# Optimization experiments

Hardware: AMD Instinct MI355X
Metric: run time of the kernel (lower is better)

Reference implementation:

```python
import jax, jax.numpy as jnp
import numpy as np

B, H, M, HS = 256, 1024, 256, 128  # batch, hidden=entry_size, mem_cap, head_size
TAU = 1.0
sg = jax.lax.stop_gradient


def _gumbel(u):
    # torch: -log(1e-20 - log(1e-20 + rand))
    return -jnp.log(1e-20 - jnp.log(1e-20 + u))


def _hard_gumbel_softmax(scores, u, tau):
    # straight-through hard gumbel softmax over the memcap axis (axis=1)
    y = jax.nn.softmax((scores + sg(_gumbel(u))) * tau, axis=1)
    ymax = jnp.max(y, axis=1, keepdims=True)
    hard = (y == ymax).astype(y.dtype)
    return sg(hard - y) + y


def setup_inputs() -> dict:
    key = jax.random.key(0)
    ks = jax.random.split(key, 20)
    stdv = 1.0 / np.sqrt(H)
    U = lambda k, shp: jax.random.uniform(k, shp, jnp.float32, -stdv, stdv)
    inp = {
        'input_': jax.random.normal(ks[0], (B, H), jnp.float32),
        'h_0': jax.random.normal(ks[1], (B, H), jnp.float32),
        'mem': jnp.zeros((B, M, H), jnp.float32),
        'last_usage': jnp.full((B, M), -99999.0, jnp.float32),
        'u1': jax.random.uniform(ks[2], (B, M), jnp.float32),
        'u2': jax.random.uniform(ks[3], (B, M), jnp.float32),
        'W_ih': U(ks[4], (H, 3 * H)),
        'W_hh': U(ks[5], (H, 3 * H)),
        'W_rh': U(ks[6], (H, 3 * H)),
        'W_s1': U(ks[7], (H, H)),
        'W_s2': U(ks[8], (H, H)),
        'W_s3': U(ks[9], (H, H)),
        'bias': jnp.zeros((1, 3 * H), jnp.float32),
        'W_im': U(ks[10], (H, HS + 1)),
        'W_hm': U(ks[11], (H, HS + 1)),
        'fc1_w': U(ks[12], (HS, H)),
        'fc1_b': jnp.zeros((HS,), jnp.float32),
        'W_im1': U(ks[13], (H, HS + 1)),
        'W_hm1': U(ks[14], (H, HS + 1)),
        'W_mm1': U(ks[15], (H, HS + 1)),
        'bias_m1': jnp.zeros((1, HS + 1), jnp.float32),
        'bias_1': jnp.zeros((1, H), jnp.float32),
        'bias_2': jnp.zeros((1, H), jnp.float32),
        'bias_3': jnp.zeros((1, H), jnp.float32),
    }
    return inp


def reference(input_, h_0, mem, last_usage, u1, u2,
              W_ih, W_hh, W_rh, W_s1, W_s2, W_s3, bias,
              W_im, W_hm, fc1_w, fc1_b,
              W_im1, W_hm1, W_mm1, bias_m1, bias_1, bias_2, bias_3):
    memcap = mem.shape[1]
    hidden = h_0.shape[1]
    # write: memcnt == 0 -> one-hot write index at slot 0, broadcast over batch
    widx = jnp.zeros((1, memcap), mem.dtype).at[0, 0].set(1.0)
    ones = widx[:, :, None]                       # (1, M, 1)
    mem = h_0[:, None, :] * ones + mem * (1.0 - ones)  # (B, M, E)
    last_use = jax.nn.sigmoid(sg(last_usage))     # (B, M), detached
    # addressing head (computed on detached input/h_0/mem, as in torch)
    read_head = jnp.tanh(sg(input_) @ W_im + sg(h_0) @ W_hm)          # (B, HS+1)
    head_vecs = jnp.concatenate(
        [sg(mem) @ fc1_w.T + fc1_b, last_use[:, :, None]], axis=2)    # (B, M, HS+1)
    scores = jnp.einsum('bh,bmh->bm', read_head, head_vecs)
    y1 = _hard_gumbel_softmax(scores, u1, TAU)
    entry = jnp.einsum('bm,bme->be', y1, mem)     # (B, E)
    # GRU-like gating
    w_b = jax.nn.sigmoid(entry @ W_rh + h_0 @ W_hh + input_ @ W_ih + bias)
    r, z, n = jnp.split(w_b, 3, axis=1)
    h_new = jnp.tanh(input_ @ W_s1 + bias_1 + r * (h_0 @ W_s2 + bias_2)
                     + z * (bias_3 + entry @ W_s3))
    # second read head (not detached)
    head1 = jnp.tanh(input_ @ W_im1 + h_0 @ W_hm1 + entry @ W_mm1 + bias_m1)
    scores1 = jnp.einsum('bh,bmh->bm', head1, head_vecs)
    y2 = _hard_gumbel_softmax(scores1, u2, TAU)
    entry_o = jnp.einsum('bm,bme->be', y2, mem)
    h_1 = n * h_new + (1.0 - n) * h_0
    o = jnp.concatenate([h_1, entry_o], axis=1)
    return (h_1, o)
```

## Files before the change

### kernel.cpp

```cpp
#include <hip/hip_runtime.h>

#define BB 256
#define HH 1024
#define MM 256
#define HS 128
#define NH 129

typedef __attribute__((ext_vector_type(8))) short short8;
typedef __attribute__((ext_vector_type(4))) float float4v;

__device__ __forceinline__ float sigmoidf_(float x) { return 1.0f / (1.0f + expf(-x)); }
__device__ __forceinline__ float gumbelf_(float u) { return -logf(1e-20f - logf(1e-20f + u)); }

__device__ __forceinline__ unsigned short f2bf(float x) {
    union { float f; unsigned u; } c; c.f = x;
    unsigned u = c.u;
    return (unsigned short)((u + 0x7FFFu + ((u >> 16) & 1u)) >> 16);
}

__global__ __launch_bounds__(256) void k_cvt_w(const float* __restrict__ W_ih,
                                               const float* __restrict__ W_hh,
                                               const float* __restrict__ W_rh,
                                               const float* __restrict__ W_s1,
                                               const float* __restrict__ W_s2,
                                               const float* __restrict__ W_s3,
                                               unsigned short* __restrict__ WtG,
                                               unsigned short* __restrict__ WtS) {
    __shared__ unsigned short T[64][66];
    int bx = blockIdx.x;
    const float* src;
    unsigned short* dst;
    int k0, n0, sstr, dstr, krel;
    if (bx < 2304) {
        int kt = bx / 48, nt = bx % 48;
        k0 = kt * 64; n0 = nt * 64;
        src = (k0 < 1024) ? W_ih : (k0 < 2048) ? W_hh : W_rh;
        krel = k0 & 1023;
        dst = WtG; sstr = 3072; dstr = 3072;
    } else {
        int r = bx - 2304;
        int seg = r >> 8;
        int rem = r & 255;
        int kt = rem >> 4, nt = rem & 15;
        k0 = kt * 64; n0 = nt * 64;
        src = (seg == 0) ? W_s1 : (seg == 1) ? W_s2 : W_s3;
        krel = k0;
        dst = WtS + (size_t)seg * 1048576; sstr = 1024; dstr = 1024;
    }
    int t = threadIdx.x;
    for (int i = 0; i < 4; ++i) {
        int e = i * 256 + t;
        int kk = e >> 4, nn0 = (e & 15) * 4;
        float4 v = *(const float4*)(src + (size_t)(krel + kk) * sstr + n0 + nn0);
        T[nn0 + 0][kk] = f2bf(v.x);
        T[nn0 + 1][kk] = f2bf(v.y);
        T[nn0 + 2][kk] = f2bf(v.z);
        T[nn0 + 3][kk] = f2bf(v.w);
    }
    __syncthreads();
    for (int i = 0; i < 8; ++i) {
        int e = i * 256 + t;
        int nn = e >> 5, kk2 = (e & 31) * 2;
        unsigned val = (unsigned)T[nn][kk2] | ((unsigned)T[nn][kk2 + 1] << 16);
        *(unsigned*)(dst + (size_t)(n0 + nn) * dstr + k0 + kk2) = val;
    }
}

__global__ __launch_bounds__(1024) void k_score1(const float* __restrict__ input_,
                                                 const float* __restrict__ h0,
                                                 const float* __restrict__ W_im,
                                                 const float* __restrict__ W_hm,
                                                 const float* __restrict__ fc1_w,
                                                 const float* __restrict__ fc1_b,
                                                 const float* __restrict__ mem,
                                                 const float* __restrict__ last_usage,
                                                 const float* __restrict__ u1,
                                                 unsigned short* __restrict__ Abf,
                                                 float* __restrict__ sg_out) {
    __shared__ float sx[HH], sh[HH], sv[HH];
    __shared__ float red[8][128];
    __shared__ float red2[8];
    __shared__ float sj[NH];
    __shared__ float scb;
    int b = blockIdx.x, t = threadIdx.x;
    if (t < 256) {
        float4 v = *(const float4*)(input_ + (size_t)b * HH + t * 4);
        *(float4*)(sx + t * 4) = v;
        ushort4 o; o.x = f2bf(v.x); o.y = f2bf(v.y); o.z = f2bf(v.z); o.w = f2bf(v.w);
        *(ushort4*)(Abf + (size_t)b * 3072 + t * 4) = o;
    } else if (t < 512) {
        int tt = t - 256;
        float4 v = *(const float4*)(h0 + (size_t)b * HH + tt * 4);
        *(float4*)(sh + tt * 4) = v;
        ushort4 o; o.x = f2bf(v.x); o.y = f2bf(v.y); o.z = f2bf(v.z); o.w = f2bf(v.w);
        *(ushort4*)(Abf + (size_t)b * 3072 + 1024 + tt * 4) = o;
    }
    __syncthreads();
    {
        int j = t & 127, ks = t >> 7;
        int hb = ks * 128;
        float p = 0.f;
#pragma unroll 8
        for (int h = hb; h < hb + 128; ++h)
            p += sx[h] * W_im[h * NH + j] + sh[h] * W_hm[h * NH + j];
        red[ks][j] = p;
        if (t >= 1016) {
            int k2 = t - 1016;
            int hb2 = k2 * 128;
            float q = 0.f;
#pragma unroll 8
            for (int h = hb2; h < hb2 + 128; ++h)
                q += sx[h] * W_im[h * NH + 128] + sh[h] * W_hm[h * NH + 128];
            red2[k2] = q;
        }
    }
    __syncthreads();
    if (t < 128) {
        float s = 0.f;
        for (int k = 0; k < 8; ++k) s += red[k][t];
        sj[t] = tanhf(s);
    } else if (t == 128) {
        float s = 0.f;
        for (int k = 0; k < 8; ++k) s += red2[k];
        sj[128] = tanhf(s);
    }
    __syncthreads();
    {
        float acc = 0.f;
#pragma unroll 4
        for (int j = 0; j < HS; ++j) acc += sj[j] * fc1_w[(size_t)j * HH + t];
        sv[t] = acc;
    }
    if (t < 64) {
        float p = sj[t] * fc1_b[t] + sj[t + 64] * fc1_b[t + 64];
        for (int off = 32; off > 0; off >>= 1) p += __shfl_down(p, off, 64);
        if (t == 0) scb = p;
    }
    __syncthreads();
    float cb = scb, hf = sj[128];
    int wave = t >> 6, lane = t & 63;
    float4 rv[4];
#pragma unroll
    for (int it = 0; it < 4; ++it) rv[it] = *(const float4*)(sv + it * 256 + lane * 4);
    for (int i = 0; i < 16; ++i) {
        int m = wave * 16 + i;
        const float* row = (m == 0) ? (h0 + (size_t)b * HH) : (mem + ((size_t)(b * MM + m)) * HH);
        float p = 0.f;
#pragma unroll
        for (int it = 0; it < 4; ++it) {
            float4 mv = *(const float4*)(row + it * 256 + lane * 4);
            p += mv.x * rv[it].x + mv.y * rv[it].y + mv.z * rv[it].z + mv.w * rv[it].w;
        }
        for (int off = 32; off > 0; off >>= 1) p += __shfl_down(p, off, 64);
        if (lane == 0) {
            float lu = sigmoidf_(last_usage[b * MM + m]);
            sg_out[b * MM + m] = p + cb + hf * lu + gumbelf_(u1[b * MM + m]);
        }
    }
}

__global__ __launch_bounds__(1024) void k_sel_score2(const float* __restrict__ sg1,
                                                     const float* __restrict__ mem,
                                                     const float* __restrict__ h0,
                                                     const float* __restrict__ input_,
                                                     const float* __restrict__ W_im1,
                                                     const float* __restrict__ W_hm1,
                                                     const float* __restrict__ W_mm1,
                                                     const float* __restrict__ bias_m1,
                                                     const float* __restrict__ fc1_w,
                                                     const float* __restrict__ fc1_b,
                                                     const float* __restrict__ last_usage,
                                                     const float* __restrict__ u2,
                                                     unsigned short* __restrict__ Abf,
                                                     float* __restrict__ sg_out) {
    __shared__ float svals[256];
    __shared__ int sidx[256];
    __shared__ float sx[HH], sh[HH], se[HH], sv[HH];
    __shared__ float red[8][128];
    __shared__ float red2[8];
    __shared__ float sj[NH];
    __shared__ float scb;
    int b = blockIdx.x, t = threadIdx.x;
    if (t < 256) {
        svals[t] = sg1[b * MM + t];
        sidx[t] = t;
    }
    __syncthreads();
    for (int s = 128; s > 0; s >>= 1) {
        if (t < s) {
            if (svals[t + s] > svals[t]) { svals[t] = svals[t + s]; sidx[t] = sidx[t + s]; }
        }
        __syncthreads();
    }
    int mstar = sidx[0];
    const float* erow = (mstar == 0) ? (h0 + (size_t)b * HH) : (mem + ((size_t)(b * MM + mstar)) * HH);
    if (t < 256) {
        float4 v = *(const float4*)(erow + t * 4);
        *(float4*)(se + t * 4) = v;
        ushort4 o; o.x = f2bf(v.x); o.y = f2bf(v.y); o.z = f2bf(v.z); o.w = f2bf(v.w);
        *(ushort4*)(Abf + (size_t)b * 3072 + 2048 + t * 4) = o;
    } else if (t < 512) {
        int tt = t - 256;
        *(float4*)(sx + tt * 4) = *(const float4*)(input_ + (size_t)b * HH + tt * 4);
    } else if (t < 768) {
        int tt = t - 512;
        *(float4*)(sh + tt * 4) = *(const float4*)(h0 + (size_t)b * HH + tt * 4);
    }
    __syncthreads();
    {
        int j = t & 127, ks = t >> 7;
        int hb = ks * 128;
        float p = 0.f;
#pragma unroll 4
        for (int h = hb; h < hb + 128; ++h)
            p += sx[h] * W_im1[h * NH + j] + sh[h] * W_hm1[h * NH + j] + se[h] * W_mm1[h * NH + j];
        red[ks][j] = p;
        if (t >= 1016) {
            int k2 = t - 1016;
            int hb2 = k2 * 128;
            float q = 0.f;
#pragma unroll 4
            for (int h = hb2; h < hb2 + 128; ++h)
                q += sx[h] * W_im1[h * NH + 128] + sh[h] * W_hm1[h * NH + 128] + se[h] * W_mm1[h * NH + 128];
            red2[k2] = q;
        }
    }
    __syncthreads();
    if (t < 128) {
        float s = bias_m1[t];
        for (int k = 0; k < 8; ++k) s += red[k][t];
        sj[t] = tanhf(s);
    } else if (t == 128) {
        float s = bias_m1[128];
        for (int k = 0; k < 8; ++k) s += red2[k];
        sj[128] = tanhf(s);
    }
    __syncthreads();
    {
        float acc = 0.f;
#pragma unroll 4
        for (int j = 0; j < HS; ++j) acc += sj[j] * fc1_w[(size_t)j * HH + t];
        sv[t] = acc;
    }
    if (t < 64) {
        float p = sj[t] * fc1_b[t] + sj[t + 64] * fc1_b[t + 64];
        for (int off = 32; off > 0; off >>= 1) p += __shfl_down(p, off, 64);
        if (t == 0) scb = p;
    }
    __syncthreads();
    float cb = scb, hf = sj[128];
    int wave = t >> 6, lane = t & 63;
    float4 rv[4];
#pragma unroll
    for (int it = 0; it < 4; ++it) rv[it] = *(const float4*)(sv + it * 256 + lane * 4);
    for (int i = 0; i < 16; ++i) {
        int m = wave * 16 + i;
        const float* row = (m == 0) ? (h0 + (size_t)b * HH) : (mem + ((size_t)(b * MM + m)) * HH);
        float p = 0.f;
#pragma unroll
        for (int it = 0; it < 4; ++it) {
            float4 mv = *(const float4*)(row + it * 256 + lane * 4);
            p += mv.x * rv[it].x + mv.y * rv[it].y + mv.z * rv[it].z + mv.w * rv[it].w;
        }
        for (int off = 32; off > 0; off >>= 1) p += __shfl_down(p, off, 64);
        if (lane == 0) {
            float lu = sigmoidf_(last_usage[b * MM + m]);
            sg_out[b * MM + m] = p + cb + hf * lu + gumbelf_(u2[b * MM + m]);
        }
    }
}

__global__ __launch_bounds__(256) void k_gemm(const unsigned short* __restrict__ Abf,
                                              const unsigned short* __restrict__ WtG,
                                              const unsigned short* __restrict__ WtS,
                                              float* __restrict__ wbp,
                                              float* __restrict__ Sp) {
    __shared__ unsigned short As[128 * 72];
    __shared__ unsigned short Bs[128 * 72];
    int bx = blockIdx.x;
    int mtile = bx & 1, unit = bx >> 1;
    int m0 = mtile * 128;
    const unsigned short* Bp;
    const unsigned short* Ap;
    float* pout;
    int bstr, ncol0;
    if (unit < 144) {
        int nt = unit % 24;
        int kidx = unit / 24;
        int ksel = kidx >> 1, khalf = kidx & 1;
        ncol0 = nt * 128;
        Bp = WtG + (size_t)ncol0 * 3072 + ksel * 1024 + khalf * 512;
        bstr = 3072;
        Ap = Abf + ksel * 1024 + khalf * 512;
        pout = wbp + (size_t)kidx * 786432;
    } else {
        int su = unit - 144;
        int seg = su / 16;
        int rem = su % 16;
        int khalf = rem >> 3, nts = rem & 7;
        ncol0 = seg * 1024 + nts * 128;
        Bp = WtS + (size_t)seg * 1048576 + (size_t)(nts * 128) * 1024 + khalf * 512;
        bstr = 1024;
        Ap = Abf + seg * 1024 + khalf * 512;
        pout = Sp + (size_t)khalf * 786432;
    }

    int tid = threadIdx.x;
    int wave = tid >> 6, lane = tid & 63;
    int wm = wave >> 1, wn = wave & 1;
    int q = lane >> 4, lm = lane & 15;

    float4v acc[4][4];
    for (int i = 0; i < 4; ++i)
        for (int j = 0; j < 4; ++j)
            acc[i][j] = (float4v){0.f, 0.f, 0.f, 0.f};

    for (int kt = 0; kt < 512; kt += 64) {
        for (int rr = 0; rr < 4; ++rr) {
            int e = rr * 256 + tid;
            int row = e >> 3, cg = e & 7;
            *(uint4*)&As[row * 72 + cg * 8] =
                *(const uint4*)(Ap + (size_t)(m0 + row) * 3072 + kt + cg * 8);
            *(uint4*)&Bs[row * 72 + cg * 8] =
                *(const uint4*)(Bp + (size_t)row * bstr + kt + cg * 8);
        }
        __syncthreads();
        for (int ks = 0; ks < 64; ks += 32) {
            short8 av[4], bv[4];
            for (int i = 0; i < 4; ++i)
                av[i] = *(const short8*)&As[(wm * 64 + i * 16 + lm) * 72 + ks + q * 8];
            for (int j = 0; j < 4; ++j)
                bv[j] = *(const short8*)&Bs[(wn * 64 + j * 16 + lm) * 72 + ks + q * 8];
            for (int i = 0; i < 4; ++i)
                for (int j = 0; j < 4; ++j)
                    acc[i][j] = __builtin_amdgcn_mfma_f32_16x16x32_bf16(av[i], bv[j], acc[i][j], 0, 0, 0);
        }
        __syncthreads();
    }

    for (int i = 0; i < 4; ++i)
        for (int j = 0; j < 4; ++j) {
            int n = ncol0 + wn * 64 + j * 16 + lm;
            for (int reg = 0; reg < 4; ++reg) {
                int m = m0 + wm * 64 + i * 16 + q * 4 + reg;
                pout[(size_t)m * 3072 + n] = acc[i][j][reg];
            }
        }
}

__global__ __launch_bounds__(256) void k_final(const float* __restrict__ sg2,
                                               const float* __restrict__ mem,
                                               const float* __restrict__ wbp,
                                               const float* __restrict__ Sp,
                                               const float* __restrict__ h0,
                                               const float* __restrict__ bias,
                                               const float* __restrict__ b1,
                                               const float* __restrict__ b2,
                                               const float* __restrict__ b3,
                                               float* __restrict__ out) {
    __shared__ float svals[256];
    __shared__ int sidx[256];
    int b = blockIdx.x, t = threadIdx.x;
    svals[t] = sg2[b * MM + t];
    sidx[t] = t;
    __syncthreads();
    for (int s = 128; s > 0; s >>= 1) {
        if (t < s) {
            if (svals[t + s] > svals[t]) { svals[t] = svals[t + s]; sidx[t] = sidx[t + s]; }
        }
        __syncthreads();
    }
    int mstar = sidx[0];
    const float* erow = (mstar == 0) ? (h0 + (size_t)b * HH) : (mem + ((size_t)(b * MM + mstar)) * HH);
    float* o_row = out + (size_t)BB * HH + (size_t)b * 2 * HH;
    {
        int hb = t * 4;
        *(float4*)(o_row + HH + hb) = *(const float4*)(erow + hb);
    }
    int h = t * 4;
    size_t base = (size_t)b * 3072;
// ... 53 lines not shown
    const float* h0 = (const float*)d_in[1];
    const float* mem = (const float*)d_in[2];
    const float* last_usage = (const float*)d_in[3];
    const float* u1 = (const float*)d_in[4];
    const float* u2 = (const float*)d_in[5];
    const float* W_ih = (const float*)d_in[6];
    const float* W_hh = (const float*)d_in[7];
    const float* W_rh = (const float*)d_in[8];
    const float* W_s1 = (const float*)d_in[9];
    const float* W_s2 = (const float*)d_in[10];
    const float* W_s3 = (const float*)d_in[11];
    const float* bias = (const float*)d_in[12];
    const float* W_im = (const float*)d_in[13];
    const float* W_hm = (const float*)d_in[14];
    const float* fc1_w = (const float*)d_in[15];
    const float* fc1_b = (const float*)d_in[16];
    const float* W_im1 = (const float*)d_in[17];
    const float* W_hm1 = (const float*)d_in[18];
    const float* W_mm1 = (const float*)d_in[19];
    const float* bias_m1 = (const float*)d_in[20];
    const float* bias_1 = (const float*)d_in[21];
    const float* bias_2 = (const float*)d_in[22];
    const float* bias_3 = (const float*)d_in[23];
    float* out = (float*)d_out;

    float* ws = (float*)d_ws;
    float* sg1 = ws;
    float* sg2 = sg1 + 65536;
    float* wbp = sg2 + 65536;
    float* Sp = wbp + 6 * 786432;
    unsigned short* Abf = (unsigned short*)(Sp + 2 * 786432);
    unsigned short* WtG = Abf + 786432;
    unsigned short* WtS = WtG + 9437184;

    k_cvt_w<<<3072, 256, 0, stream>>>(W_ih, W_hh, W_rh, W_s1, W_s2, W_s3, WtG, WtS);
    k_score1<<<BB, 1024, 0, stream>>>(input_, h0, W_im, W_hm, fc1_w, fc1_b,
                                      mem, last_usage, u1, Abf, sg1);
    k_sel_score2<<<BB, 1024, 0, stream>>>(sg1, mem, h0, input_, W_im1, W_hm1, W_mm1, bias_m1,
                                          fc1_w, fc1_b, last_usage, u2, Abf, sg2);
    k_gemm<<<384, 256, 0, stream>>>(Abf, WtG, WtS, wbp, Sp);
    k_final<<<BB, 256, 0, stream>>>(sg2, mem, wbp, Sp, h0, bias, bias_1, bias_2, bias_3, out);
}
```

Before: 595.9 us.

## Fuse weight conversion with score1 and overlap input/h0 GEMMs with score2

Merges the bf16 weight transpose-conversion into the first scoring kernel as extra blocks, so both run in one launch. The second-scoring kernel also carries the GEMM tiles for the input and h0 K-slices, which do not depend on the selected entry, so they run alongside the selection work. Only the entry-dependent K-slices stay in a smaller follow-up GEMM launch. Scoring blocks shrink from 1024 to 256 threads with more work per thread, which cuts per-block parallelism in exchange for co-scheduling. There is a risk that the phase-2 GEMM blocks read WtG/WtS right after phase 1 writes them, but they are in separate launches on the same stream, so ordering holds.

```diff
diff --git a/kernel.cpp b/kernel.cpp
--- a/kernel.cpp
+++ b/kernel.cpp
@@ -18,293 +18,11 @@
     return (unsigned short)((u + 0x7FFFu + ((u >> 16) & 1u)) >> 16);
 }
 
-__global__ __launch_bounds__(256) void k_cvt_w(const float* __restrict__ W_ih,
-                                               const float* __restrict__ W_hh,
-                                               const float* __restrict__ W_rh,
-                                               const float* __restrict__ W_s1,
-                                               const float* __restrict__ W_s2,
-                                               const float* __restrict__ W_s3,
-                                               unsigned short* __restrict__ WtG,
-                                               unsigned short* __restrict__ WtS) {
-    __shared__ unsigned short T[64][66];
-    int bx = blockIdx.x;
-    const float* src;
-    unsigned short* dst;
-    int k0, n0, sstr, dstr, krel;
-    if (bx < 2304) {
-        int kt = bx / 48, nt = bx % 48;
-        k0 = kt * 64; n0 = nt * 64;
-        src = (k0 < 1024) ? W_ih : (k0 < 2048) ? W_hh : W_rh;
-        krel = k0 & 1023;
-        dst = WtG; sstr = 3072; dstr = 3072;
-    } else {
-        int r = bx - 2304;
-        int seg = r >> 8;
-        int rem = r & 255;
-        int kt = rem >> 4, nt = rem & 15;
-        k0 = kt * 64; n0 = nt * 64;
-        src = (seg == 0) ? W_s1 : (seg == 1) ? W_s2 : W_s3;
-        krel = k0;
-        dst = WtS + (size_t)seg * 1048576; sstr = 1024; dstr = 1024;
-    }
-    int t = threadIdx.x;
-    for (int i = 0; i < 4; ++i) {
-        int e = i * 256 + t;
-        int kk = e >> 4, nn0 = (e & 15) * 4;
-        float4 v = *(const float4*)(src + (size_t)(krel + kk) * sstr + n0 + nn0);
-        T[nn0 + 0][kk] = f2bf(v.x);
-        T[nn0 + 1][kk] = f2bf(v.y);
-        T[nn0 + 2][kk] = f2bf(v.z);
-        T[nn0 + 3][kk] = f2bf(v.w);
-    }
-    __syncthreads();
-    for (int i = 0; i < 8; ++i) {
-        int e = i * 256 + t;
-        int nn = e >> 5, kk2 = (e & 31) * 2;
-        unsigned val = (unsigned)T[nn][kk2] | ((unsigned)T[nn][kk2 + 1] << 16);
-        *(unsigned*)(dst + (size_t)(n0 + nn) * dstr + k0 + kk2) = val;
-    }
-}
-
-__global__ __launch_bounds__(1024) void k_score1(const float* __restrict__ input_,
-                                                 const float* __restrict__ h0,
-                                                 const float* __restrict__ W_im,
-                                                 const float* __restrict__ W_hm,
-                                                 const float* __restrict__ fc1_w,
-                                                 const float* __restrict__ fc1_b,
-                                                 const float* __restrict__ mem,
-                                                 const float* __restrict__ last_usage,
-                                                 const float* __restrict__ u1,
-                                                 unsigned short* __restrict__ Abf,
-                                                 float* __restrict__ sg_out) {
-    __shared__ float sx[HH], sh[HH], sv[HH];
-    __shared__ float red[8][128];
-    __shared__ float red2[8];
-    __shared__ float sj[NH];
-    __shared__ float scb;
-    int b = blockIdx.x, t = threadIdx.x;
-    if (t < 256) {
-        float4 v = *(const float4*)(input_ + (size_t)b * HH + t * 4);
-        *(float4*)(sx + t * 4) = v;
-        ushort4 o; o.x = f2bf(v.x); o.y = f2bf(v.y); o.z = f2bf(v.z); o.w = f2bf(v.w);
-        *(ushort4*)(Abf + (size_t)b * 3072 + t * 4) = o;
-    } else if (t < 512) {
-        int tt = t - 256;
-        float4 v = *(const float4*)(h0 + (size_t)b * HH + tt * 4);
-        *(float4*)(sh + tt * 4) = v;
-        ushort4 o; o.x = f2bf(v.x); o.y = f2bf(v.y); o.z = f2bf(v.z); o.w = f2bf(v.w);
-        *(ushort4*)(Abf + (size_t)b * 3072 + 1024 + tt * 4) = o;
-    }
-    __syncthreads();
-    {
-        int j = t & 127, ks = t >> 7;
-        int hb = ks * 128;
-        float p = 0.f;
-#pragma unroll 8
-        for (int h = hb; h < hb + 128; ++h)
-            p += sx[h] * W_im[h * NH + j] + sh[h] * W_hm[h * NH + j];
-        red[ks][j] = p;
-        if (t >= 1016) {
-            int k2 = t - 1016;
-            int hb2 = k2 * 128;
-            float q = 0.f;
-#pragma unroll 8
-            for (int h = hb2; h < hb2 + 128; ++h)
-                q += sx[h] * W_im[h * NH + 128] + sh[h] * W_hm[h * NH + 128];
-            red2[k2] = q;
-        }
-    }
-    __syncthreads();
-    if (t < 128) {
-        float s = 0.f;
-        for (int k = 0; k < 8; ++k) s += red[k][t];
-        sj[t] = tanhf(s);
-    } else if (t == 128) {
-        float s = 0.f;
-        for (int k = 0; k < 8; ++k) s += red2[k];
-        sj[128] = tanhf(s);
-    }
-    __syncthreads();
-    {
-        float acc = 0.f;
-#pragma unroll 4
-        for (int j = 0; j < HS; ++j) acc += sj[j] * fc1_w[(size_t)j * HH + t];
-        sv[t] = acc;
-    }
-    if (t < 64) {
-        float p = sj[t] * fc1_b[t] + sj[t + 64] * fc1_b[t + 64];
-        for (int off = 32; off > 0; off >>= 1) p += __shfl_down(p, off, 64);
-        if (t == 0) scb = p;
-    }
-    __syncthreads();
-    float cb = scb, hf = sj[128];
-    int wave = t >> 6, lane = t & 63;
-    float4 rv[4];
-#pragma unroll
-    for (int it = 0; it < 4; ++it) rv[it] = *(const float4*)(sv + it * 256 + lane * 4);
-    for (int i = 0; i < 16; ++i) {
-        int m = wave * 16 + i;
-        const float* row = (m == 0) ? (h0 + (size_t)b * HH) : (mem + ((size_t)(b * MM + m)) * HH);
-        float p = 0.f;
-#pragma unroll
-        for (int it = 0; it < 4; ++it) {
-            float4 mv = *(const float4*)(row + it * 256 + lane * 4);
-            p += mv.x * rv[it].x + mv.y * rv[it].y + mv.z * rv[it].z + mv.w * rv[it].w;
-        }
-        for (int off = 32; off > 0; off >>= 1) p += __shfl_down(p, off, 64);
-        if (lane == 0) {
-            float lu = sigmoidf_(last_usage[b * MM + m]);
-            sg_out[b * MM + m] = p + cb + hf * lu + gumbelf_(u1[b * MM + m]);
-        }
-    }
-}
-
-__global__ __launch_bounds__(1024) void k_sel_score2(const float* __restrict__ sg1,
-                                                     const float* __restrict__ mem,
-                                                     const float* __restrict__ h0,
-                                                     const float* __restrict__ input_,
-                                                     const float* __restrict__ W_im1,
-                                                     const float* __restrict__ W_hm1,
-                                                     const float* __restrict__ W_mm1,
-                                                     const float* __restrict__ bias_m1,
-                                                     const float* __restrict__ fc1_w,
-                                                     const float* __restrict__ fc1_b,
-                                                     const float* __restrict__ last_usage,
-                                                     const float* __restrict__ u2,
-                                                     unsigned short* __restrict__ Abf,
-                                                     float* __restrict__ sg_out) {
-    __shared__ float svals[256];
-    __shared__ int sidx[256];
-    __shared__ float sx[HH], sh[HH], se[HH], sv[HH];
-    __shared__ float red[8][128];
-    __shared__ float red2[8];
-    __shared__ float sj[NH];
-    __shared__ float scb;
-    int b = blockIdx.x, t = threadIdx.x;
-    if (t < 256) {
-        svals[t] = sg1[b * MM + t];
-        sidx[t] = t;
-    }
-    __syncthreads();
-    for (int s = 128; s > 0; s >>= 1) {
-        if (t < s) {
-            if (svals[t + s] > svals[t]) { svals[t] = svals[t + s]; sidx[t] = sidx[t + s]; }
-        }
-        __syncthreads();
-    }
-    int mstar = sidx[0];
-    const float* erow = (mstar == 0) ? (h0 + (size_t)b * HH) : (mem + ((size_t)(b * MM + mstar)) * HH);
-    if (t < 256) {
-        float4 v = *(const float4*)(erow + t * 4);
-        *(float4*)(se + t * 4) = v;
-        ushort4 o; o.x = f2bf(v.x); o.y = f2bf(v.y); o.z = f2bf(v.z); o.w = f2bf(v.w);
-        *(ushort4*)(Abf + (size_t)b * 3072 + 2048 + t * 4) = o;
-    } else if (t < 512) {
-        int tt = t - 256;
-        *(float4*)(sx + tt * 4) = *(const float4*)(input_ + (size_t)b * HH + tt * 4);
-    } else if (t < 768) {
-        int tt = t - 512;
-        *(float4*)(sh + tt * 4) = *(const float4*)(h0 + (size_t)b * HH + tt * 4);
-    }
-    __syncthreads();
-    {
-        int j = t & 127, ks = t >> 7;
-        int hb = ks * 128;
-        float p = 0.f;
-#pragma unroll 4
-        for (int h = hb; h < hb + 128; ++h)
-            p += sx[h] * W_im1[h * NH + j] + sh[h] * W_hm1[h * NH + j] + se[h] * W_mm1[h * NH + j];
-        red[ks][j] = p;
-        if (t >= 1016) {
-            int k2 = t - 1016;
-            int hb2 = k2 * 128;
-            float q = 0.f;
-#pragma unroll 4
-            for (int h = hb2; h < hb2 + 128; ++h)
-                q += sx[h] * W_im1[h * NH + 128] + sh[h] * W_hm1[h * NH + 128] + se[h] * W_mm1[h * NH + 128];
-            red2[k2] = q;
-        }
-    }
-    __syncthreads();
-    if (t < 128) {
-        float s = bias_m1[t];
-        for (int k = 0; k < 8; ++k) s += red[k][t];
-        sj[t] = tanhf(s);
-    } else if (t == 128) {
-        float s = bias_m1[128];
-        for (int k = 0; k < 8; ++k) s += red2[k];
-        sj[128] = tanhf(s);
-    }
-    __syncthreads();
-    {
-        float acc = 0.f;
-#pragma unroll 4
-        for (int j = 0; j < HS; ++j) acc += sj[j] * fc1_w[(size_t)j * HH + t];
-        sv[t] = acc;
-    }
-    if (t < 64) {
-        float p = sj[t] * fc1_b[t] + sj[t + 64] * fc1_b[t + 64];
-        for (int off = 32; off > 0; off >>= 1) p += __shfl_down(p, off, 64);
-        if (t == 0) scb = p;
-    }
-    __syncthreads();
-    float cb = scb, hf = sj[128];
-    int wave = t >> 6, lane = t & 63;
-    float4 rv[4];
-#pragma unroll
-    for (int it = 0; it < 4; ++it) rv[it] = *(const float4*)(sv + it * 256 + lane * 4);
-    for (int i = 0; i < 16; ++i) {
-        int m = wave * 16 + i;
-        const float* row = (m == 0) ? (h0 + (size_t)b * HH) : (mem + ((size_t)(b * MM + m)) * HH);
-        float p = 0.f;
-#pragma unroll
-        for (int it = 0; it < 4; ++it) {
-            float4 mv = *(const float4*)(row + it * 256 + lane * 4);
-            p += mv.x * rv[it].x + mv.y * rv[it].y + mv.z * rv[it].z + mv.w * rv[it].w;
-        }
-        for (int off = 32; off > 0; off >>= 1) p += __shfl_down(p, off, 64);
-        if (lane == 0) {
-            float lu = sigmoidf_(last_usage[b * MM + m]);
-            sg_out[b * MM + m] = p + cb + hf * lu + gumbelf_(u2[b * MM + m]);
-        }
-    }
-}
-
-__global__ __launch_bounds__(256) void k_gemm(const unsigned short* __restrict__ Abf,
-                                              const unsigned short* __restrict__ WtG,
-                                              const unsigned short* __restrict__ WtS,
-                                              float* __restrict__ wbp,
-                                              float* __restrict__ Sp) {
-    __shared__ unsigned short As[128 * 72];
-    __shared__ unsigned short Bs[128 * 72];
-    int bx = blockIdx.x;
-    int mtile = bx & 1, unit = bx >> 1;
-    int m0 = mtile * 128;
-    const unsigned short* Bp;
-    const unsigned short* Ap;
-    float* pout;
-    int bstr, ncol0;
-    if (unit < 144) {
-        int nt = unit % 24;
-        int kidx = unit / 24;
-        int ksel = kidx >> 1, khalf = kidx & 1;
-        ncol0 = nt * 128;
-        Bp = WtG + (size_t)ncol0 * 3072 + ksel * 1024 + khalf * 512;
-        bstr = 3072;
-        Ap = Abf + ksel * 1024 + khalf * 512;
-        pout = wbp + (size_t)kidx * 786432;
-    } else {
-        int su = unit - 144;
-        int seg = su / 16;
-        int rem = su % 16;
-        int khalf = rem >> 3, nts = rem & 7;
-        ncol0 = seg * 1024 + nts * 128;
-        Bp = WtS + (size_t)seg * 1048576 + (size_t)(nts * 128) * 1024 + khalf * 512;
-        bstr = 1024;
-        Ap = Abf + seg * 1024 + khalf * 512;
-        pout = Sp + (size_t)khalf * 786432;
-    }
-
+__device__ __forceinline__ void gemm_unit(const unsigned short* __restrict__ Ap,
+                                          const unsigned short* __restrict__ Bp,
+                                          int bstr, int m0, int ncol0,
+                                          float* __restrict__ pout,
+                                          unsigned short* As, unsigned short* Bs) {
     int tid = threadIdx.x;
     int wave = tid >> 6, lane = tid & 63;
     int wm = wave >> 1, wn = wave & 1;
@@ -346,6 +64,322 @@
                 pout[(size_t)m * 3072 + n] = acc[i][j][reg];
             }
         }
+}
+
+__global__ __launch_bounds__(256) void k_phase1(const float* __restrict__ input_,
+                                                const float* __restrict__ h0,
+                                                const float* __restrict__ W_im,
+                                                const float* __restrict__ W_hm,
+                                                const float* __restrict__ fc1_w,
+                                                const float* __restrict__ fc1_b,
+                                                const float* __restrict__ mem,
+                                                const float* __restrict__ last_usage,
+                                                const float* __restrict__ u1,
+                                                const float* __restrict__ W_ih,
+                                                const float* __restrict__ W_hh,
+                                                const float* __restrict__ W_rh,
+                                                const float* __restrict__ W_s1,
+                                                const float* __restrict__ W_s2,
+                                                const float* __restrict__ W_s3,
+                                                unsigned short* __restrict__ Abf,
+                                                unsigned short* __restrict__ WtG,
+                                                unsigned short* __restrict__ WtS,
+                                                float* __restrict__ sg_out) {
+    __shared__ __align__(16) unsigned char smem[14400];
+    int bx = blockIdx.x, t = threadIdx.x;
+    if (bx >= 256) {
+        unsigned short (*T)[66] = (unsigned short (*)[66])smem;
+        int tile = bx - 256;
+        const float* src;
+        unsigned short* dst;
+        int k0, n0, sstr, dstr, krel;
+        if (tile < 2304) {
+            int kt = tile / 48, nt = tile % 48;
+            k0 = kt * 64; n0 = nt * 64;
+            src = (k0 < 1024) ? W_ih : (k0 < 2048) ? W_hh : W_rh;
+            krel = k0 & 1023;
+            dst = WtG; sstr = 3072; dstr = 3072;
+        } else {
+            int r = tile - 2304;
+            int seg = r >> 8;
+            int rem = r & 255;
+            int kt = rem >> 4, nt = rem & 15;
+            k0 = kt * 64; n0 = nt * 64;
+            src = (seg == 0) ? W_s1 : (seg == 1) ? W_s2 : W_s3;
+            krel = k0;
+            dst = WtS + (size_t)seg * 1048576; sstr = 1024; dstr = 1024;
+        }
+        for (int i = 0; i < 4; ++i) {
+            int e = i * 256 + t;
+            int kk = e >> 4, nn0 = (e & 15) * 4;
+            float4 v = *(const float4*)(src + (size_t)(krel + kk) * sstr + n0 + nn0);
+            T[nn0 + 0][kk] = f2bf(v.x);
+            T[nn0 + 1][kk] = f2bf(v.y);
+            T[nn0 + 2][kk] = f2bf(v.z);
+            T[nn0 + 3][kk] = f2bf(v.w);
+        }
+        __syncthreads();
+        for (int i = 0; i < 8; ++i) {
+            int e = i * 256 + t;
+            int nn = e >> 5, kk2 = (e & 31) * 2;
+            unsigned val = (unsigned)T[nn][kk2] | ((unsigned)T[nn][kk2 + 1] << 16);
+            *(unsigned*)(dst + (size_t)(n0 + nn) * dstr + k0 + kk2) = val;
+        }
+        return;
+    }
+    float* sx = (float*)smem;
+    float* sh = sx + 1024;
+    float* sv = sh + 1024;
+    float* red = sv + 1024;
+    float* red2 = red + 256;
+    float* sj = red2 + 2;
+    float* scb = sj + 129;
+    int b = bx;
+    {
+        float4 vx = *(const float4*)(input_ + (size_t)b * HH + t * 4);
+        *(float4*)(sx + t * 4) = vx;
+        ushort4 o; o.x = f2bf(vx.x); o.y = f2bf(vx.y); o.z = f2bf(vx.z); o.w = f2bf(vx.w);
+        *(ushort4*)(Abf + (size_t)b * 3072 + t * 4) = o;
+        float4 vh = *(const float4*)(h0 + (size_t)b * HH + t * 4);
+        *(float4*)(sh + t * 4) = vh;
+        ushort4 p; p.x = f2bf(vh.x); p.y = f2bf(vh.y); p.z = f2bf(vh.z); p.w = f2bf(vh.w);
+        *(ushort4*)(Abf + (size_t)b * 3072 + 1024 + t * 4) = p;
+    }
+    __syncthreads();
+    {
+        int j = t & 127, ks = t >> 7;
+        int hb = ks * 512;
+        float p = 0.f;
+#pragma unroll 8
+        for (int h = hb; h < hb + 512; ++h)
+            p += sx[h] * W_im[h * NH + j] + sh[h] * W_hm[h * NH + j];
+        red[ks * 128 + j] = p;
+        if (t >= 254) {
+            int k2 = t - 254;
+            int hb2 = k2 * 512;
+            float q = 0.f;
+#pragma unroll 8
+            for (int h = hb2; h < hb2 + 512; ++h)
+                q += sx[h] * W_im[h * NH + 128] + sh[h] * W_hm[h * NH + 128];
+            red2[k2] = q;
+        }
+    }
+    __syncthreads();
+    if (t < 128) sj[t] = tanhf(red[t] + red[128 + t]);
+    else if (t == 128) sj[128] = tanhf(red2[0] + red2[1]);
+    __syncthreads();
+    {
+        float a0 = 0.f, a1 = 0.f, a2 = 0.f, a3 = 0.f;
+#pragma unroll 4
+        for (int j = 0; j < HS; ++j) {
+            float s = sj[j];
+            const float* w = fc1_w + (size_t)j * HH + t;
+            a0 += s * w[0]; a1 += s * w[256]; a2 += s * w[512]; a3 += s * w[768];
+        }
+        sv[t] = a0; sv[t + 256] = a1; sv[t + 512] = a2; sv[t + 768] = a3;
+    }
+    if (t < 64) {
+        float p = sj[t] * fc1_b[t] + sj[t + 64] * fc1_b[t + 64];
+        for (int off = 32; off > 0; off >>= 1) p += __shfl_down(p, off, 64);
+        if (t == 0) *scb = p;
+    }
+    __syncthreads();
+    float cb = *scb, hf = sj[128];
+    int wave = t >> 6, lane = t & 63;
+    float4 rv[4];
+#pragma unroll
+    for (int it = 0; it < 4; ++it) rv[it] = *(const float4*)(sv + it * 256 + lane * 4);
+    for (int i = 0; i < 64; ++i) {
+        int m = wave * 64 + i;
+        const float* row = (m == 0) ? (h0 + (size_t)b * HH) : (mem + ((size_t)(b * MM + m)) * HH);
+        float p = 0.f;
+#pragma unroll
+        for (int it = 0; it < 4; ++it) {
+            float4 mv = *(const float4*)(row + it * 256 + lane * 4);
+            p += mv.x * rv[it].x + mv.y * rv[it].y + mv.z * rv[it].z + mv.w * rv[it].w;
+        }
+        for (int off = 32; off > 0; off >>= 1) p += __shfl_down(p, off, 64);
+        if (lane == 0) {
+            float lu = sigmoidf_(last_usage[b * MM + m]);
+            sg_out[b * MM + m] = p + cb + hf * lu + gumbelf_(u1[b * MM + m]);
+        }
+    }
+}
+
+__global__ __launch_bounds__(256) void k_phase2(const float* __restrict__ sg1,
+                                                const float* __restrict__ mem,
+                                                const float* __restrict__ h0,
+                                                const float* __restrict__ input_,
+                                                const float* __restrict__ W_im1,
+                                                const float* __restrict__ W_hm1,
+                                                const float* __restrict__ W_mm1,
+                                                const float* __restrict__ bias_m1,
+                                                const float* __restrict__ fc1_w,
+                                                const float* __restrict__ fc1_b,
+                                                const float* __restrict__ last_usage,
+                                                const float* __restrict__ u2,
+                                                unsigned short* __restrict__ Abf,
+                                                const unsigned short* __restrict__ WtG,
+                                                const unsigned short* __restrict__ WtS,
+                                                float* __restrict__ wbp,
+                                                float* __restrict__ Sp,
+                                                float* __restrict__ sg_out) {
+    __shared__ __align__(16) unsigned char smem[36864];
+    int bx = blockIdx.x, t = threadIdx.x;
+    if (bx >= 256) {
+        unsigned short* As = (unsigned short*)smem;
+        unsigned short* Bs = As + 128 * 72;
+        int inst = bx - 256;
+        int mtile = inst & 1, u = inst >> 1;
+        int m0 = mtile * 128;
+        const unsigned short* Ap;
+        const unsigned short* Bp;
+        float* pout;
+        int bstr, ncol0;
+        if (u < 96) {
+            int nt = u % 24, kidx = u / 24;
+            int ksel = kidx >> 1, khalf = kidx & 1;
+            ncol0 = nt * 128;
+            Bp = WtG + (size_t)ncol0 * 3072 + ksel * 1024 + khalf * 512;
+            bstr = 3072;
+            Ap = Abf + ksel * 1024 + khalf * 512;
+            pout = wbp + (size_t)kidx * 786432;
+        } else {
+            int su = u - 96;
+            int seg = su >> 4, rem = su & 15;
+            int khalf = rem >> 3, nts = rem & 7;
+            ncol0 = seg * 1024 + nts * 128;
+            Bp = WtS + (size_t)seg * 1048576 + (size_t)(nts * 128) * 1024 + khalf * 512;
+            bstr = 1024;
+            Ap = Abf + seg * 1024 + khalf * 512;
+            pout = Sp + (size_t)khalf * 786432;
+        }
+        gemm_unit(Ap, Bp, bstr, m0, ncol0, pout, As, Bs);
+        return;
+    }
+    float* sx = (float*)smem;
+    float* sh = sx + 1024;
+    float* se = sh + 1024;
+    float* sv = se + 1024;
+    float* svals = sv + 1024;
+    int* sidx = (int*)(svals + 256);
+    float* red = (float*)(sidx + 256);
+    float* red2 = red + 256;
+    float* sj = red2 + 2;
+    float* scb = sj + 129;
+    int b = bx;
+    svals[t] = sg1[b * MM + t];
+    sidx[t] = t;
+    __syncthreads();
+    for (int s = 128; s > 0; s >>= 1) {
+        if (t < s) {
+            if (svals[t + s] > svals[t]) { svals[t] = svals[t + s]; sidx[t] = sidx[t + s]; }
+        }
+        __syncthreads();
+    }
+    int mstar = sidx[0];
+    const float* erow = (mstar == 0) ? (h0 + (size_t)b * HH) : (mem + ((size_t)(b * MM + mstar)) * HH);
+    {
+        float4 e = *(const float4*)(erow + t * 4);
+        *(float4*)(se + t * 4) = e;
+        ushort4 o; o.x = f2bf(e.x); o.y = f2bf(e.y); o.z = f2bf(e.z); o.w = f2bf(e.w);
+        *(ushort4*)(Abf + (size_t)b * 3072 + 2048 + t * 4) = o;
+        *(float4*)(sx + t * 4) = *(const float4*)(input_ + (size_t)b * HH + t * 4);
+        *(float4*)(sh + t * 4) = *(const float4*)(h0 + (size_t)b * HH + t * 4);
+    }
+    __syncthreads();
+    {
+        int j = t & 127, ks = t >> 7;
+        int hb = ks * 512;
+        float p = 0.f;
+#pragma unroll 4
+        for (int h = hb; h < hb + 512; ++h)
+            p += sx[h] * W_im1[h * NH + j] + sh[h] * W_hm1[h * NH + j] + se[h] * W_mm1[h * NH + j];
+        red[ks * 128 + j] = p;
+        if (t >= 254) {
+            int k2 = t - 254;
+            int hb2 = k2 * 512;
+            float q = 0.f;
+#pragma unroll 4
+            for (int h = hb2; h < hb2 + 512; ++h)
+                q += sx[h] * W_im1[h * NH + 128] + sh[h] * W_hm1[h * NH + 128] + se[h] * W_mm1[h * NH + 128];
+            red2[k2] = q;
+        }
+    }
+    __syncthreads();
+    if (t < 128) sj[t] = tanhf(bias_m1[t] + red[t] + red[128 + t]);
+    else if (t == 128) sj[128] = tanhf(bias_m1[128] + red2[0] + red2[1]);
+    __syncthreads();
+    {
+        float a0 = 0.f, a1 = 0.f, a2 = 0.f, a3 = 0.f;
+#pragma unroll 4
+        for (int j = 0; j < HS; ++j) {
+            float s = sj[j];
+            const float* w = fc1_w + (size_t)j * HH + t;
+            a0 += s * w[0]; a1 += s * w[256]; a2 += s * w[512]; a3 += s * w[768];
+        }
+        sv[t] = a0; sv[t + 256] = a1; sv[t + 512] = a2; sv[t + 768] = a3;
+    }
+    if (t < 64) {
+        float p = sj[t] * fc1_b[t] + sj[t + 64] * fc1_b[t + 64];
+        for (int off = 32; off > 0; off >>= 1) p += __shfl_down(p, off, 64);
+        if (t == 0) *scb = p;
+    }
+    __syncthreads();
+    float cb = *scb, hf = sj[128];
+    int wave = t >> 6, lane = t & 63;
+    float4 rv[4];
+#pragma unroll
+    for (int it = 0; it < 4; ++it) rv[it] = *(const float4*)(sv + it * 256 + lane * 4);
+    for (int i = 0; i < 64; ++i) {
+        int m = wave * 64 + i;
+        const float* row = (m == 0) ? (h0 + (size_t)b * HH) : (mem + ((size_t)(b * MM + m)) * HH);
+        float p = 0.f;
+#pragma unroll
+        for (int it = 0; it < 4; ++it) {
+            float4 mv = *(const float4*)(row + it * 256 + lane * 4);
+            p += mv.x * rv[it].x + mv.y * rv[it].y + mv.z * rv[it].z + mv.w * rv[it].w;
+        }
+        for (int off = 32; off > 0; off >>= 1) p += __shfl_down(p, off, 64);
+        if (lane == 0) {
+            float lu = sigmoidf_(last_usage[b * MM + m]);
+            sg_out[b * MM + m] = p + cb + hf * lu + gumbelf_(u2[b * MM + m]);
+        }
+    }
+}
+
+__global__ __launch_bounds__(256) void k_gemm2(const unsigned short* __restrict__ Abf,
+                                               const unsigned short* __restrict__ WtG,
+                                               const unsigned short* __restrict__ WtS,
+                                               float* __restrict__ wbp,
+                                               float* __restrict__ Sp) {
+    __shared__ unsigned short As[128 * 72];
+    __shared__ unsigned short Bs[128 * 72];
+    int bx = blockIdx.x;
+    int mtile = bx & 1, u = bx >> 1;
+    int m0 = mtile * 128;
+    const unsigned short* Ap;
+    const unsigned short* Bp;
+    float* pout;
+    int bstr, ncol0;
+    if (u < 48) {
+        int nt = u % 24, khalf = u / 24;
+        int kidx = 4 + khalf;
+        ncol0 = nt * 128;
+        Bp = WtG + (size_t)ncol0 * 3072 + 2048 + khalf * 512;
+        bstr = 3072;
+        Ap = Abf + 2048 + khalf * 512;
+        pout = wbp + (size_t)kidx * 786432;
+    } else {
+        int su = u - 48;
+        int khalf = su >> 3, nts = su & 7;
+        ncol0 = 2048 + nts * 128;
+        Bp = WtS + (size_t)2 * 1048576 + (size_t)(nts * 128) * 1024 + khalf * 512;
+        bstr = 1024;
+        Ap = Abf + 2048 + khalf * 512;
+        pout = Sp + (size_t)khalf * 786432;
+    }
+    gemm_unit(Ap, Bp, bstr, m0, ncol0, pout, As, Bs);
 }
 
 __global__ __launch_bounds__(256) void k_final(const float* __restrict__ sg2,
@@ -466,11 +500,13 @@
     unsigned short* WtG = Abf + 786432;
     unsigned short* WtS = WtG + 9437184;
 
-    k_cvt_w<<<3072, 256, 0, stream>>>(W_ih, W_hh, W_rh, W_s1, W_s2, W_s3, WtG, WtS);
-    k_score1<<<BB, 1024, 0, stream>>>(input_, h0, W_im, W_hm, fc1_w, fc1_b,
-                                      mem, last_usage, u1, Abf, sg1);
-    k_sel_score2<<<BB, 1024, 0, stream>>>(sg1, mem, h0, input_, W_im1, W_hm1, W_mm1, bias_m1,
-                                          fc1_w, fc1_b, last_usage, u2, Abf, sg2);
-    k_gemm<<<384, 256, 0, stream>>>(Abf, WtG, WtS, wbp, Sp);
+    k_phase1<<<256 + 3072, 256, 0, stream>>>(input_, h0, W_im, W_hm, fc1_w, fc1_b,
+                                             mem, last_usage, u1,
+                                             W_ih, W_hh, W_rh, W_s1, W_s2, W_s3,
+                                             Abf, WtG, WtS, sg1);
+    k_phase2<<<512, 256, 0, stream>>>(sg1, mem, h0, input_, W_im1, W_hm1, W_mm1, bias_m1,
+                                      fc1_w, fc1_b, last_usage, u2,
+                                      Abf, WtG, WtS, wbp, Sp, sg2);
+    k_gemm2<<<128, 256, 0, stream>>>(Abf, WtG, WtS, wbp, Sp);
     k_final<<<BB, 256, 0, stream>>>(sg2, mem, wbp, Sp, h0, bias, bias_1, bias_2, bias_3, out);
 }
```

New measurement: 763.4 us. 1.28x slower.

## Precompute mem@fc1_w^T with a bf16 MFMA GEMM and score from it

Applied to the files above, without the earlier changes.

Reassociates the addressing score: instead of projecting each read head through fc1_w and dotting it with full 1024-wide memory rows, it computes P = mem @ fc1_w^T once with a bf16 MFMA GEMM. Both score kernels then take 128-wide dot products against P, and the write-slot row (h0) is handled separately. The goal is to stop streaming the whole memory tensor twice, since the score kernels are bandwidth-bound. The P GEMM is fused into the weight-conversion launch as extra blocks. The cost is a bf16 rounding of mem and fc1_w in the scores, which could flip the hard argmax selection, plus an extra P buffer in the workspace.

```diff
diff --git a/kernel.cpp b/kernel.cpp
--- a/kernel.cpp
+++ b/kernel.cpp
@@ -18,52 +18,160 @@
     return (unsigned short)((u + 0x7FFFu + ((u >> 16) & 1u)) >> 16);
 }
 
-__global__ __launch_bounds__(256) void k_cvt_w(const float* __restrict__ W_ih,
-                                               const float* __restrict__ W_hh,
-                                               const float* __restrict__ W_rh,
-                                               const float* __restrict__ W_s1,
-                                               const float* __restrict__ W_s2,
-                                               const float* __restrict__ W_s3,
-                                               unsigned short* __restrict__ WtG,
-                                               unsigned short* __restrict__ WtS) {
-    __shared__ unsigned short T[64][66];
-    int bx = blockIdx.x;
-    const float* src;
-    unsigned short* dst;
-    int k0, n0, sstr, dstr, krel;
-    if (bx < 2304) {
-        int kt = bx / 48, nt = bx % 48;
-        k0 = kt * 64; n0 = nt * 64;
-        src = (k0 < 1024) ? W_ih : (k0 < 2048) ? W_hh : W_rh;
-        krel = k0 & 1023;
-        dst = WtG; sstr = 3072; dstr = 3072;
-    } else {
-        int r = bx - 2304;
-        int seg = r >> 8;
-        int rem = r & 255;
-        int kt = rem >> 4, nt = rem & 15;
-        k0 = kt * 64; n0 = nt * 64;
-        src = (seg == 0) ? W_s1 : (seg == 1) ? W_s2 : W_s3;
-        krel = k0;
-        dst = WtS + (size_t)seg * 1048576; sstr = 1024; dstr = 1024;
-    }
-    int t = threadIdx.x;
-    for (int i = 0; i < 4; ++i) {
-        int e = i * 256 + t;
-        int kk = e >> 4, nn0 = (e & 15) * 4;
-        float4 v = *(const float4*)(src + (size_t)(krel + kk) * sstr + n0 + nn0);
-        T[nn0 + 0][kk] = f2bf(v.x);
-        T[nn0 + 1][kk] = f2bf(v.y);
-        T[nn0 + 2][kk] = f2bf(v.z);
-        T[nn0 + 3][kk] = f2bf(v.w);
-    }
-    __syncthreads();
-    for (int i = 0; i < 8; ++i) {
-        int e = i * 256 + t;
-        int nn = e >> 5, kk2 = (e & 31) * 2;
-        unsigned val = (unsigned)T[nn][kk2] | ((unsigned)T[nn][kk2 + 1] << 16);
-        *(unsigned*)(dst + (size_t)(n0 + nn) * dstr + k0 + kk2) = val;
-    }
+__device__ __forceinline__ void score_from_P(const float* __restrict__ P,
+                                             const float* __restrict__ sj,
+                                             const float* __restrict__ sv,
+                                             const float* __restrict__ h0row,
+                                             float cb, float hf,
+                                             const float* __restrict__ last_usage,
+                                             const float* __restrict__ u,
+                                             float* __restrict__ sg_out,
+                                             int b, int t) {
+    int wave = t >> 6, lane = t & 63;
+    int mrow = wave * 16 + (lane >> 2);
+    int q4 = lane & 3;
+    const float* Prow = P + ((size_t)b * MM + mrow) * HS + q4 * 32;
+    float p = 0.f;
+#pragma unroll
+    for (int g = 0; g < 8; ++g) {
+        float4 pv = *(const float4*)(Prow + g * 4);
+        float4 sjv = *(const float4*)(sj + q4 * 32 + g * 4);
+        p += pv.x * sjv.x + pv.y * sjv.y + pv.z * sjv.z + pv.w * sjv.w;
+    }
+    p += __shfl_down(p, 2, 64);
+    p += __shfl_down(p, 1, 64);
+    if (q4 == 0 && mrow != 0) {
+        int mb = b * MM + mrow;
+        sg_out[mb] = p + cb + hf * sigmoidf_(last_usage[mb]) + gumbelf_(u[mb]);
+    }
+    if (wave == 15) {
+        float q = 0.f;
+#pragma unroll
+        for (int it = 0; it < 4; ++it) {
+            float4 mv = *(const float4*)(h0row + it * 256 + lane * 4);
+            float4 rv = *(const float4*)(sv + it * 256 + lane * 4);
+            q += mv.x * rv.x + mv.y * rv.y + mv.z * rv.z + mv.w * rv.w;
+        }
+        for (int off = 32; off > 0; off >>= 1) q += __shfl_down(q, off, 64);
+        if (lane == 0) {
+            int mb = b * MM;
+            sg_out[mb] = q + cb + hf * sigmoidf_(last_usage[mb]) + gumbelf_(u[mb]);
+        }
+    }
+}
+
+__global__ __launch_bounds__(256) void k_pgemm_cvt(const float* __restrict__ mem,
+                                                   const float* __restrict__ fc1_w,
+                                                   const float* __restrict__ W_ih,
+                                                   const float* __restrict__ W_hh,
+                                                   const float* __restrict__ W_rh,
+                                                   const float* __restrict__ W_s1,
+                                                   const float* __restrict__ W_s2,
+                                                   const float* __restrict__ W_s3,
+                                                   unsigned short* __restrict__ WtG,
+                                                   unsigned short* __restrict__ WtS,
+                                                   float* __restrict__ P) {
+    __shared__ __align__(16) unsigned char smem[73728];
+    int bx = blockIdx.x, t = threadIdx.x;
+    if (bx >= 512) {
+        unsigned short (*T)[66] = (unsigned short (*)[66])smem;
+        int tile = bx - 512;
+        const float* src;
+        unsigned short* dst;
+        int k0, n0, sstr, dstr, krel;
+        if (tile < 2304) {
+            int kt = tile / 48, nt = tile % 48;
+            k0 = kt * 64; n0 = nt * 64;
+            src = (k0 < 1024) ? W_ih : (k0 < 2048) ? W_hh : W_rh;
+            krel = k0 & 1023;
+            dst = WtG; sstr = 3072; dstr = 3072;
+        } else {
+            int r = tile - 2304;
+            int seg = r >> 8;
+            int rem = r & 255;
+            int kt = rem >> 4, nt = rem & 15;
+            k0 = kt * 64; n0 = nt * 64;
+            src = (seg == 0) ? W_s1 : (seg == 1) ? W_s2 : W_s3;
+            krel = k0;
+            dst = WtS + (size_t)seg * 1048576; sstr = 1024; dstr = 1024;
+        }
+        for (int i = 0; i < 4; ++i) {
+            int e = i * 256 + t;
+            int kk = e >> 4, nn0 = (e & 15) * 4;
+            float4 v = *(const float4*)(src + (size_t)(krel + kk) * sstr + n0 + nn0);
+            T[nn0 + 0][kk] = f2bf(v.x);
+            T[nn0 + 1][kk] = f2bf(v.y);
+            T[nn0 + 2][kk] = f2bf(v.z);
+            T[nn0 + 3][kk] = f2bf(v.w);
+        }
+        __syncthreads();
+        for (int i = 0; i < 8; ++i) {
+            int e = i * 256 + t;
+            int nn = e >> 5, kk2 = (e & 31) * 2;
+            unsigned val = (unsigned)T[nn][kk2] | ((unsigned)T[nn][kk2 + 1] << 16);
+            *(unsigned*)(dst + (size_t)(n0 + nn) * dstr + k0 + kk2) = val;
+        }
+        return;
+    }
+    unsigned short* As = (unsigned short*)smem;
+    unsigned short* Bs = As + 128 * 72;
+    int m0 = bx * 128;
+    const float* Asrc = mem + (size_t)m0 * 1024;
+
+    int wave = t >> 6, lane = t & 63;
+    int wm = wave >> 1, wn = wave & 1;
+    int q = lane >> 4, lm = lane & 15;
+
+    float4v acc[4][4];
+    for (int i = 0; i < 4; ++i)
+        for (int j = 0; j < 4; ++j)
+            acc[i][j] = (float4v){0.f, 0.f, 0.f, 0.f};
+
+    for (int kt = 0; kt < 1024; kt += 64) {
+        for (int g = 0; g < 4; ++g) {
+            int gi = g * 256 + t;
+            int row = gi >> 3, seg = gi & 7;
+            const float* sa = Asrc + (size_t)row * 1024 + kt + seg * 8;
+            float4 f0 = *(const float4*)sa;
+            float4 f1 = *(const float4*)(sa + 4);
+            uint4 pk;
+            pk.x = (unsigned)f2bf(f0.x) | ((unsigned)f2bf(f0.y) << 16);
+            pk.y = (unsigned)f2bf(f0.z) | ((unsigned)f2bf(f0.w) << 16);
+            pk.z = (unsigned)f2bf(f1.x) | ((unsigned)f2bf(f1.y) << 16);
+            pk.w = (unsigned)f2bf(f1.z) | ((unsigned)f2bf(f1.w) << 16);
+            *(uint4*)&As[row * 72 + seg * 8] = pk;
+            const float* sb = fc1_w + (size_t)row * 1024 + kt + seg * 8;
+            float4 g0 = *(const float4*)sb;
+            float4 g1 = *(const float4*)(sb + 4);
+            uint4 qk;
+            qk.x = (unsigned)f2bf(g0.x) | ((unsigned)f2bf(g0.y) << 16);
+            qk.y = (unsigned)f2bf(g0.z) | ((unsigned)f2bf(g0.w) << 16);
+            qk.z = (unsigned)f2bf(g1.x) | ((unsigned)f2bf(g1.y) << 16);
+            qk.w = (unsigned)f2bf(g1.z) | ((unsigned)f2bf(g1.w) << 16);
+            *(uint4*)&Bs[row * 72 + seg * 8] = qk;
+        }
+        __syncthreads();
+        for (int ks = 0; ks < 64; ks += 32) {
+            short8 av[4], bv[4];
+            for (int i = 0; i < 4; ++i)
+                av[i] = *(const short8*)&As[(wm * 64 + i * 16 + lm) * 72 + ks + q * 8];
+            for (int j = 0; j < 4; ++j)
+                bv[j] = *(const short8*)&Bs[(wn * 64 + j * 16 + lm) * 72 + ks + q * 8];
+            for (int i = 0; i < 4; ++i)
+                for (int j = 0; j < 4; ++j)
+                    acc[i][j] = __builtin_amdgcn_mfma_f32_16x16x32_bf16(av[i], bv[j], acc[i][j], 0, 0, 0);
+        }
+        __syncthreads();
+    }
+
+    for (int i = 0; i < 4; ++i)
+        for (int j = 0; j < 4; ++j) {
+            int n = wn * 64 + j * 16 + lm;
+            for (int reg = 0; reg < 4; ++reg) {
+                int m = m0 + wm * 64 + i * 16 + q * 4 + reg;
+                P[(size_t)m * HS + n] = acc[i][j][reg];
+            }
+        }
 }
 
 __global__ __launch_bounds__(1024) void k_score1(const float* __restrict__ input_,
@@ -72,15 +180,17 @@
                                                  const float* __restrict__ W_hm,
                                                  const float* __restrict__ fc1_w,
                                                  const float* __restrict__ fc1_b,
-                                                 const float* __restrict__ mem,
+                                                 const float* __restrict__ P,
                                                  const float* __restrict__ last_usage,
                                                  const float* __restrict__ u1,
                                                  unsigned short* __restrict__ Abf,
                                                  float* __restrict__ sg_out) {
-    __shared__ float sx[HH], sh[HH], sv[HH];
+    __shared__ __align__(16) float sx[HH];
+    __shared__ __align__(16) float sh[HH];
+    __shared__ __align__(16) float sv[HH];
     __shared__ float red[8][128];
     __shared__ float red2[8];
-    __shared__ float sj[NH];
+    __shared__ __align__(16) float sj[132];
     __shared__ float scb;
     int b = blockIdx.x, t = threadIdx.x;
     if (t < 256) {
@@ -137,26 +247,7 @@
         if (t == 0) scb = p;
     }
     __syncthreads();
-    float cb = scb, hf = sj[128];
-    int wave = t >> 6, lane = t & 63;
-    float4 rv[4];
-#pragma unroll
-    for (int it = 0; it < 4; ++it) rv[it] = *(const float4*)(sv + it * 256 + lane * 4);
-    for (int i = 0; i < 16; ++i) {
-        int m = wave * 16 + i;
-        const float* row = (m == 0) ? (h0 + (size_t)b * HH) : (mem + ((size_t)(b * MM + m)) * HH);
-        float p = 0.f;
-#pragma unroll
-        for (int it = 0; it < 4; ++it) {
-            float4 mv = *(const float4*)(row + it * 256 + lane * 4);
-            p += mv.x * rv[it].x + mv.y * rv[it].y + mv.z * rv[it].z + mv.w * rv[it].w;
-        }
-        for (int off = 32; off > 0; off >>= 1) p += __shfl_down(p, off, 64);
-        if (lane == 0) {
-            float lu = sigmoidf_(last_usage[b * MM + m]);
-            sg_out[b * MM + m] = p + cb + hf * lu + gumbelf_(u1[b * MM + m]);
-        }
-    }
+    score_from_P(P, sj, sv, h0 + (size_t)b * HH, scb, sj[128], last_usage, u1, sg_out, b, t);
 }
 
 __global__ __launch_bounds__(1024) void k_sel_score2(const float* __restrict__ sg1,
@@ -169,16 +260,20 @@
                                                      const float* __restrict__ bias_m1,
                                                      const float* __restrict__ fc1_w,
                                                      const float* __restrict__ fc1_b,
+                                                     const float* __restrict__ P,
                                                      const float* __restrict__ last_usage,
                                                      const float* __restrict__ u2,
                                                      unsigned short* __restrict__ Abf,
                                                      float* __restrict__ sg_out) {
     __shared__ float svals[256];
     __shared__ int sidx[256];
-    __shared__ float sx[HH], sh[HH], se[HH], sv[HH];
+    __shared__ __align__(16) float sx[HH];
+    __shared__ __align__(16) float sh[HH];
+    __shared__ __align__(16) float se[HH];
+    __shared__ __align__(16) float sv[HH];
     __shared__ float red[8][128];
     __shared__ float red2[8];
-    __shared__ float sj[NH];
+    __shared__ __align__(16) float sj[132];
     __shared__ float scb;
     int b = blockIdx.x, t = threadIdx.x;
     if (t < 256) {
@@ -248,26 +343,7 @@
         if (t == 0) scb = p;
     }
     __syncthreads();
-    float cb = scb, hf = sj[128];
-    int wave = t >> 6, lane = t & 63;
-    float4 rv[4];
-#pragma unroll
-    for (int it = 0; it < 4; ++it) rv[it] = *(const float4*)(sv + it * 256 + lane * 4);
-    for (int i = 0; i < 16; ++i) {
-        int m = wave * 16 + i;
-        const float* row = (m == 0) ? (h0 + (size_t)b * HH) : (mem + ((size_t)(b * MM + m)) * HH);
-        float p = 0.f;
-#pragma unroll
-        for (int it = 0; it < 4; ++it) {
-            float4 mv = *(const float4*)(row + it * 256 + lane * 4);
-            p += mv.x * rv[it].x + mv.y * rv[it].y + mv.z * rv[it].z + mv.w * rv[it].w;
-        }
-        for (int off = 32; off > 0; off >>= 1) p += __shfl_down(p, off, 64);
-        if (lane == 0) {
-            float lu = sigmoidf_(last_usage[b * MM + m]);
-            sg_out[b * MM + m] = p + cb + hf * lu + gumbelf_(u2[b * MM + m]);
-        }
-    }
+    score_from_P(P, sj, sv, h0 + (size_t)b * HH, scb, sj[128], last_usage, u2, sg_out, b, t);
 }
 
 __global__ __launch_bounds__(256) void k_gemm(const unsigned short* __restrict__ Abf,
@@ -465,12 +541,14 @@
     unsigned short* Abf = (unsigned short*)(Sp + 2 * 786432);
     unsigned short* WtG = Abf + 786432;
     unsigned short* WtS = WtG + 9437184;
-
-    k_cvt_w<<<3072, 256, 0, stream>>>(W_ih, W_hh, W_rh, W_s1, W_s2, W_s3, WtG, WtS);
+    float* Pbuf = (float*)(WtS + 3145728);
+
+    k_pgemm_cvt<<<512 + 3072, 256, 0, stream>>>(mem, fc1_w, W_ih, W_hh, W_rh,
+                                                W_s1, W_s2, W_s3, WtG, WtS, Pbuf);
     k_score1<<<BB, 1024, 0, stream>>>(input_, h0, W_im, W_hm, fc1_w, fc1_b,
-                                      mem, last_usage, u1, Abf, sg1);
+                                      Pbuf, last_usage, u1, Abf, sg1);
     k_sel_score2<<<BB, 1024, 0, stream>>>(sg1, mem, h0, input_, W_im1, W_hm1, W_mm1, bias_m1,
-                                          fc1_w, fc1_b, last_usage, u2, Abf, sg2);
+                                          fc1_w, fc1_b, Pbuf, last_usage, u2, Abf, sg2);
     k_gemm<<<384, 256, 0, stream>>>(Abf, WtG, WtS, wbp, Sp);
     k_final<<<BB, 256, 0, stream>>>(sg2, mem, wbp, Sp, h0, bias, bias_1, bias_2, bias_3, out);
 }
```

Result: faster. 579.7 us (-2.7%).
